# Performance work log

Hardware: AMD Instinct MI355X
Metric: run time of the kernel (lower is better)

The kernel has to match this reference:

```python
import jax, jax.numpy as jnp
import numpy as np

N, E, S, A, IN, H, OUT = 100000, 400000, 20000, 16, 32, 64, 1
NNZ_SS = 160000
CUR_T, CUR_W = 37, 3


def _gelu(x):
    return jax.nn.gelu(x, approximate=False)  # torch F.gelu default = exact erf


def _spmm(row, col, val, M, nseg):
    # sparse [nseg, K] (COO) @ dense M [K, H]
    return jax.ops.segment_sum(val[:, None] * M[col], row, num_segments=nseg)


def _seg_softmax(logits, seg, nseg):
    mx = jax.ops.segment_max(logits, seg, num_segments=nseg)
    mx = jnp.where(jnp.isfinite(mx), mx, 0.0)  # empty segments -> -inf
    ex = jnp.exp(logits - mx[seg])
    den = jax.ops.segment_sum(ex, seg, num_segments=nseg)
    return ex / (den[seg] + 1e-16)  # PyG softmax epsilon


def _gatv2(x, src, dst, eproj, Wl, bl, Wr, br, att, bias, n):
    # PyG GATv2Conv, heads=1, share_weights=False, negative_slope=0.2
    xl = x @ Wl + bl
    xr = x @ Wr + br
    m = xl[src] + xr[dst] + eproj                      # [nnz, H]
    e = jax.nn.leaky_relu(m, 0.2)
    alpha = _seg_softmax(e @ att, dst, n)              # softmax over in-edges per dst
    return jax.ops.segment_sum(alpha[:, None] * xl[src], dst, num_segments=n) + bias


def _forward(fl, edge_index, se_row, se_col, sn_row, sn_col, ss_row, ss_col, cur_t, cur_w):
    (x_rec, attr, se_val, sn_val, ss_val,
     node_embed, edge_embed, segment_embed, time_embed, week_embed,
     node_lin_W, node_lin_b, attr1_W, attr1_b, attr2_W, attr2_b,
     c1_Wl, c1_bl, c1_Wr, c1_br, c1_We, c1_att, c1_bias,
     c2_Wl, c2_bl, c2_Wr, c2_br, c2_We, c2_att, c2_bias,
     c3_Wl, c3_bl, c3_Wr, c3_br, c3_We, c3_att, c3_bias,
     lin1_W, lin1_b, lin2_W, lin2_b, out_W, out_b) = fl
    src, dst = edge_index[0], edge_index[1]
    attr_f = attr @ attr1_W + attr1_b                  # shared edge feature [E, H]
    # conv1 stack over node_embed with GELU + residual-to-initial
    h = node_embed
    pre = h
    for l in range(3):
        ep = attr_f @ c1_We[l]
        h = _gelu(_gatv2(h, src, dst, ep, c1_Wl[l], c1_bl[l], c1_Wr[l], c1_br[l], c1_att[l], c1_bias[l], N)) + pre
    # conv2 stack over projected recent features
    nf = _gelu(x_rec @ node_lin_W + node_lin_b)
    pre = nf
    for l in range(3):
        ep = attr_f @ c2_We[l]
        nf = _gelu(_gatv2(nf, src, dst, ep, c2_Wl[l], c2_bl[l], c2_Wr[l], c2_br[l], c2_att[l], c2_bias[l], N)) + pre
    # sparse segment aggregations
    x1e = _spmm(se_row, se_col, se_val, edge_embed, S)
    x2e = _spmm(se_row, se_col, se_val, attr @ attr2_W + attr2_b, S)
    x1n = _spmm(sn_row, sn_col, sn_val, h, S)
    x2n = _spmm(sn_row, sn_col, sn_val, nf, S)
    t = jnp.tile(time_embed[cur_t][None, :], (S, 1))
    w = jnp.tile(week_embed[cur_w][None, :], (S, 1))
    xf = jnp.concatenate([segment_embed, x1e, x2e, x1n, x2n, t, w], axis=1)  # [S, 7H]
    # conv3 over segment graph, edge_dim=1 (sparse values as edge attr)
    ep3 = ss_val[:, None] @ c3_We                                            # [nnz_ss, H]
    xf_gnn = _gelu(_gatv2(xf, ss_row, ss_col, ep3, c3_Wl, c3_bl, c3_Wr, c3_br, c3_att, c3_bias, S))
    # MLP head uses only lins[:-1] (as in the source)
    y = _gelu(xf @ lin1_W + lin1_b)
    y = _gelu(y @ lin2_W + lin2_b)
    out = jax.nn.sigmoid(jnp.concatenate([y, xf_gnn], axis=1) @ out_W + out_b) * 3600.0
    return out


def setup_inputs():
    key = jax.random.key(0)
    ks = jax.random.split(key, 64)
    it = iter(range(64))
    def nk():
        return ks[next(it)]
    def p(shape, s=0.05):
        return jax.random.normal(nk(), shape, jnp.float32) * s
    d = {}
    d["x_rec"] = jax.random.normal(nk(), (N, IN), jnp.float32)
    d["attr"] = jax.random.normal(nk(), (E, A), jnp.float32)
    d["se_val"] = jax.random.uniform(nk(), (E,), jnp.float32)
    d["sn_val"] = jax.random.uniform(nk(), (E,), jnp.float32)
    d["ss_val"] = jax.random.uniform(nk(), (NNZ_SS,), jnp.float32)
    d["node_embed"] = p((N, H))
    d["edge_embed"] = p((E, H))
    d["segment_embed"] = p((S, H))
    d["time_embed"] = p((96, H))
    d["week_embed"] = p((7, H))
    d["node_lin_W"] = p((IN, H)); d["node_lin_b"] = p((H,))
    d["attr1_W"] = p((A, H)); d["attr1_b"] = p((H,))
    d["attr2_W"] = p((A, H)); d["attr2_b"] = p((H,))
    for c in ("c1", "c2"):
        d[c + "_Wl"] = p((3, H, H)); d[c + "_bl"] = p((3, H))
        d[c + "_Wr"] = p((3, H, H)); d[c + "_br"] = p((3, H))
        d[c + "_We"] = p((3, H, H))
        d[c + "_att"] = p((3, H)); d[c + "_bias"] = p((3, H))
    d["c3_Wl"] = p((7 * H, H)); d["c3_bl"] = p((H,))
    d["c3_Wr"] = p((7 * H, H)); d["c3_br"] = p((H,))
    d["c3_We"] = p((1, H))
    d["c3_att"] = p((H,)); d["c3_bias"] = p((H,))
    d["lin1_W"] = p((7 * H, H)); d["lin1_b"] = p((H,))
    d["lin2_W"] = p((H, H)); d["lin2_b"] = p((H,))
    d["out_W"] = p((2 * H, OUT)); d["out_b"] = p((OUT,))
    d["edge_index"] = jax.random.randint(nk(), (2, E), 0, N)
    d["se_row"] = jax.random.randint(nk(), (E,), 0, S)
    d["se_col"] = jax.random.randint(nk(), (E,), 0, E)
    d["sn_row"] = jax.random.randint(nk(), (E,), 0, S)
    d["sn_col"] = jax.random.randint(nk(), (E,), 0, N)
    d["ss_row"] = jax.random.randint(nk(), (NNZ_SS,), 0, S)
    d["ss_col"] = jax.random.randint(nk(), (NNZ_SS,), 0, S)
    d["cur_t"] = CUR_T
    d["cur_w"] = CUR_W
    return d


def reference(x_rec, attr, se_val, sn_val, ss_val, node_embed, edge_embed, segment_embed, time_embed, week_embed, node_lin_W, node_lin_b, attr1_W, attr1_b, attr2_W, attr2_b, c1_Wl, c1_bl, c1_Wr, c1_br, c1_We, c1_att, c1_bias, c2_Wl, c2_bl, c2_Wr, c2_br, c2_We, c2_att, c2_bias, c3_Wl, c3_bl, c3_Wr, c3_br, c3_We, c3_att, c3_bias, lin1_W, lin1_b, lin2_W, lin2_b, out_W, out_b, edge_index, se_row, se_col, sn_row, sn_col, ss_row, ss_col, cur_t, cur_w):
    fl = (x_rec, attr, se_val, sn_val, ss_val, node_embed, edge_embed, segment_embed, time_embed, week_embed, node_lin_W, node_lin_b, attr1_W, attr1_b, attr2_W, attr2_b, c1_Wl, c1_bl, c1_Wr, c1_br, c1_We, c1_att, c1_bias, c2_Wl, c2_bl, c2_Wr, c2_br, c2_We, c2_att, c2_bias, c3_Wl, c3_bl, c3_Wr, c3_br, c3_We, c3_att, c3_bias, lin1_W, lin1_b, lin2_W, lin2_b, out_W, out_b)
    return _forward(fl, edge_index, se_row, se_col, sn_row, sn_col, ss_row, ss_col, cur_t, cur_w)
```

## Files before the change

kernel.cpp:

```cpp
#include <hip/hip_runtime.h>
#include <hip/hip_bf16.h>
#include <math.h>

#define DEV __device__ __forceinline__
typedef unsigned short u16;
typedef unsigned int u32;
typedef __attribute__((ext_vector_type(8))) short bf16x8;
typedef __attribute__((ext_vector_type(4))) float f32x4;

DEV float gelu_f(float x) { return 0.5f * x * (1.f + erff(x * 0.70710678118654752f)); }
DEV int rfl(int v) { return __builtin_amdgcn_readfirstlane(v); }
DEV float rflf(float v) {
  int i = __builtin_amdgcn_readfirstlane(__float_as_int(v));
  return __int_as_float(i);
}
DEV u16 f2b(float x) { __hip_bfloat16 h = __float2bfloat16(x); return *reinterpret_cast<u16*>(&h); }
DEV float b2f(u16 u) { __hip_bfloat16 h; *reinterpret_cast<u16*>(&h) = u; return __bfloat162float(h); }
DEV u32 pack2(float a, float b) { return (u32)f2b(a) | ((u32)f2b(b) << 16); }

__global__ void fill_zero(float* __restrict__ p, long n) {
  long i = (long)blockIdx.x * blockDim.x + threadIdx.x;
  long st = (long)gridDim.x * blockDim.x;
  for (; i < n; i += st) p[i] = 0.f;
}

__global__ void cvt_bf16(const float* __restrict__ src, u16* __restrict__ dst, long n) {
  long i = (long)blockIdx.x * blockDim.x + threadIdx.x;
  long st = (long)gridDim.x * blockDim.x;
  for (; i < n; i += st) dst[i] = f2b(src[i]);
}

__global__ void hist4_k(const int* __restrict__ k1, const int* __restrict__ k2,
                        const int* __restrict__ k3, const int* __restrict__ k4,
                        int E, int Z,
                        int* __restrict__ c1, int* __restrict__ c2,
                        int* __restrict__ c3, int* __restrict__ c4) {
  long total = 3L * E + Z;
  long i = (long)blockIdx.x * blockDim.x + threadIdx.x;
  long st = (long)gridDim.x * blockDim.x;
  for (; i < total; i += st) {
    if (i < E)               atomicAdd(&c1[k1[i]], 1);
    else if (i < 2L * E)     atomicAdd(&c2[k2[i - E]], 1);
    else if (i < 3L * E)     atomicAdd(&c3[k3[i - 2L * E]], 1);
    else                     atomicAdd(&c4[k4[i - 3L * E]], 1);
  }
}

__global__ __launch_bounds__(256) void scan_p1f(
    const int* __restrict__ c1, const int* __restrict__ c2,
    const int* __restrict__ c3, const int* __restrict__ c4,
    int n1, int nS, int nb1, int nbS,
    int* __restrict__ b1, int* __restrict__ b2,
    int* __restrict__ b3, int* __restrict__ b4) {
  int blk = blockIdx.x;
  const int* cnt; int* bsum; int n; int lb;
  if (blk < nb1)                { cnt = c1; bsum = b1; n = n1; lb = blk; }
  else if (blk < nb1 + nbS)     { cnt = c2; bsum = b2; n = nS; lb = blk - nb1; }
  else if (blk < nb1 + 2 * nbS) { cnt = c3; bsum = b3; n = nS; lb = blk - nb1 - nbS; }
  else                          { cnt = c4; bsum = b4; n = nS; lb = blk - nb1 - 2 * nbS; }
  __shared__ int ts[256];
  int base = lb * 1024;
  int s = 0;
  #pragma unroll
  for (int k = 0; k < 4; ++k) {
    int g = base + threadIdx.x * 4 + k;
    if (g < n) s += cnt[g];
  }
  ts[threadIdx.x] = s;
  __syncthreads();
  for (int d = 128; d; d >>= 1) {
    if (threadIdx.x < d) ts[threadIdx.x] += ts[threadIdx.x + d];
    __syncthreads();
  }
  if (threadIdx.x == 0) bsum[lb] = ts[0];
}

__global__ __launch_bounds__(256) void scan_p2f(
    int* __restrict__ b1, int* __restrict__ b2, int* __restrict__ b3, int* __restrict__ b4,
    int nb1, int nbS,
    int* __restrict__ rp1, int* __restrict__ rp2, int* __restrict__ rp3, int* __restrict__ rp4,
    int n1, int nS) {
  int g = blockIdx.x;
  int* bsum = g == 0 ? b1 : g == 1 ? b2 : g == 2 ? b3 : b4;
  int* rp   = g == 0 ? rp1 : g == 1 ? rp2 : g == 2 ? rp3 : rp4;
  int nb    = g == 0 ? nb1 : nbS;
  int n     = g == 0 ? n1 : nS;
  __shared__ int ts[256];
  int tid = threadIdx.x;
  int v = (tid < nb) ? bsum[tid] : 0;
  ts[tid] = v;
  __syncthreads();
  for (int d = 1; d < 256; d <<= 1) {
    int w = (tid >= d) ? ts[tid - d] : 0;
    __syncthreads();
    ts[tid] += w;
    __syncthreads();
  }
  if (tid < nb) bsum[tid] = (tid == 0) ? 0 : ts[tid - 1];
  if (tid == 255) rp[n] = ts[255];
}

__global__ __launch_bounds__(256) void scan_p3f(
    const int* __restrict__ c1, const int* __restrict__ c2,
    const int* __restrict__ c3, const int* __restrict__ c4,
    int n1, int nS, int nb1, int nbS,
    const int* __restrict__ b1, const int* __restrict__ b2,
    const int* __restrict__ b3, const int* __restrict__ b4,
    int* __restrict__ rp1, int* __restrict__ rp2,
    int* __restrict__ rp3, int* __restrict__ rp4,
    int* __restrict__ q1, int* __restrict__ q2,
    int* __restrict__ q3, int* __restrict__ q4) {
  int blk = blockIdx.x;
  const int* cnt; const int* bsum; int* rp; int* cursor; int n; int lb;
  if (blk < nb1)                { cnt = c1; bsum = b1; rp = rp1; cursor = q1; n = n1; lb = blk; }
  else if (blk < nb1 + nbS)     { cnt = c2; bsum = b2; rp = rp2; cursor = q2; n = nS; lb = blk - nb1; }
  else if (blk < nb1 + 2 * nbS) { cnt = c3; bsum = b3; rp = rp3; cursor = q3; n = nS; lb = blk - nb1 - nbS; }
  else                          { cnt = c4; bsum = b4; rp = rp4; cursor = q4; n = nS; lb = blk - nb1 - 2 * nbS; }
  __shared__ int ts[256];
  int base = lb * 1024;
  int tid = threadIdx.x;
  int c[4];
  int s = 0;
  #pragma unroll
  for (int k = 0; k < 4; ++k) {
    int g = base + tid * 4 + k;
    c[k] = (g < n) ? cnt[g] : 0;
    s += c[k];
  }
  ts[tid] = s;
  __syncthreads();
  for (int d = 1; d < 256; d <<= 1) {
    int w = (tid >= d) ? ts[tid - d] : 0;
    __syncthreads();
    ts[tid] += w;
    __syncthreads();
  }
  int run = bsum[lb] + ((tid == 0) ? 0 : ts[tid - 1]);
  #pragma unroll
  for (int k = 0; k < 4; ++k) {
    int g = base + tid * 4 + k;
    if (g < n) {
      rp[g] = run;
      cursor[g] = run;
      run += c[k];
    }
  }
}

__global__ void scat4_k(
    const int* __restrict__ edst, const int* __restrict__ esrc,
    const int* __restrict__ se_row, const int* __restrict__ se_col, const float* __restrict__ se_val,
    const int* __restrict__ sn_row, const int* __restrict__ sn_col, const float* __restrict__ sn_val,
    const int* __restrict__ ss_col, const int* __restrict__ ss_row, const float* __restrict__ ss_val,
    int E, int Z,
    int* __restrict__ q1, int* __restrict__ q2, int* __restrict__ q3, int* __restrict__ q4,
    int* __restrict__ src1s, int* __restrict__ eid1,
    int* __restrict__ col2s, float* __restrict__ val2s,
    int* __restrict__ col3s, float* __restrict__ val3s,
    int* __restrict__ src4s, float* __restrict__ val4s) {
  long total = 3L * E + Z;
  long i = (long)blockIdx.x * blockDim.x + threadIdx.x;
  long st = (long)gridDim.x * blockDim.x;
  for (; i < total; i += st) {
    if (i < E) {
      int p = atomicAdd(&q1[edst[i]], 1);
      src1s[p] = esrc[i]; eid1[p] = (int)i;
    } else if (i < 2L * E) {
      long j = i - E;
      int p = atomicAdd(&q2[se_row[j]], 1);
      col2s[p] = se_col[j]; val2s[p] = se_val[j];
    } else if (i < 3L * E) {
      long j = i - 2L * E;
      int p = atomicAdd(&q3[sn_row[j]], 1);
      col3s[p] = sn_col[j]; val3s[p] = sn_val[j];
    } else {
      long j = i - 3L * E;
      int p = atomicAdd(&q4[ss_col[j]], 1);
      src4s[p] = ss_row[j]; val4s[p] = ss_val[j];
    }
  }
}

__global__ __launch_bounds__(256) void compose_we(
    const float* __restrict__ a1W, const float* __restrict__ a1b,
    const float* __restrict__ c1We, const float* __restrict__ c2We,
    float* __restrict__ WEC, float* __restrict__ BEC)
{
  int l = blockIdx.x;
  const float* We = (l < 3) ? (c1We + l * 4096) : (c2We + (l - 3) * 4096);
  __shared__ float wes[4096];
  int tid = threadIdx.x;
  for (int i = tid; i < 4096; i += 256) wes[i] = We[i];
  __syncthreads();
  for (int i = tid; i < 1024; i += 256) {
    int k = i >> 6, j = i & 63;
    float s = 0.f;
    #pragma unroll 16
    for (int m = 0; m < 64; ++m) s += a1W[k * 64 + m] * wes[m * 64 + j];
    WEC[l * 1024 + i] = s;
  }
  if (tid < 64) {
    float s = 0.f;
    for (int m = 0; m < 64; ++m) s += a1b[m] * wes[m * 64 + tid];
    BEC[l * 64 + tid] = s;
  }
}

__global__ __launch_bounds__(256) void prep_wt(
    const float* __restrict__ c1Wl, const float* __restrict__ c1Wr,
    const float* __restrict__ c2Wl, const float* __restrict__ c2Wr,
    const float* __restrict__ nodeW, const float* __restrict__ c3Wl,
    const float* __restrict__ c3Wr, const float* __restrict__ lin1W,
    const float* __restrict__ lin2W, u16* __restrict__ WTS)
{
  long idx = (long)blockIdx.x * 256 + threadIdx.x;
  if (idx >= 141312) return;
  float v;
  if (idx < 49152) {
    const float* src = (idx < 12288) ? c1Wl : (idx < 24576) ? c1Wr : (idx < 36864) ? c2Wl : c2Wr;
    long loc = idx & 12287;
    long m = loc >> 12;
    int c = (int)((loc >> 6) & 63), k = (int)(loc & 63);
    v = src[m * 4096 + k * 64 + c];
  } else if (idx < 51200) {
    long loc = idx - 49152;
    int c = (int)(loc >> 5), k = (int)(loc & 31);
    v = nodeW[k * 64 + c];
  } else if (idx < 137216) {
    long base = (idx < 79872) ? 51200 : (idx < 108544) ? 79872 : 108544;
    const float* src = (idx < 79872) ? c3Wl : (idx < 108544) ? c3Wr : lin1W;
    long loc = idx - base;
    int c = (int)(loc / 448), k = (int)(loc % 448);
    v = src[k * 64 + c];
  } else {
    long loc = idx - 137216;
    int c = (int)(loc >> 6), k = (int)(loc & 63);
    v = lin2W[k * 64 + c];
  }
  WTS[idx] = f2b(v);
}

template <int ACT, bool PAIR, bool XBF, bool OBF, bool DUAL>
__global__ __launch_bounds__(256) void gemm_mfma(
    const void* __restrict__ Xv, int nrows, int K,
    const u16* __restrict__ WT1, const float* __restrict__ b1, void* __restrict__ O1v,
    const u16* __restrict__ WT2, const float* __restrict__ b2, void* __restrict__ O2v,
    const void* __restrict__ Xv2,
    const u16* __restrict__ WT3, const float* __restrict__ b3, void* __restrict__ O3v,
    const u16* __restrict__ WT4, const float* __restrict__ b4, void* __restrict__ O4v)
{
  __shared__ __align__(16) u16 xs[4096];
  __shared__ __align__(16) u16 ws1[4096];
  __shared__ __align__(16) u16 ws2[PAIR ? 4096 : 8];

  int bid = blockIdx.x;
  const void* X_ = Xv;
  const u16* w1p = WT1; const float* b1p = b1; void* o1p = O1v;
  const u16* w2p = WT2; const float* b2p = b2; void* o2p = O2v;
  if constexpr (DUAL) {
    int half = gridDim.x >> 1;
    if (bid >= half) {
      bid -= half;
      X_ = Xv2;
      w1p = WT3; b1p = b3; o1p = O3v;
      w2p = WT4; b2p = b4; o2p = O4v;
    }
  }

  const int tid = threadIdx.x;
  const int row0 = bid * 64;
  const int wid = tid >> 6, lane = tid & 63;
  const int lrow = lane & 15, lgrp = lane >> 4;
  const int r0 = wid * 16;
  const int sr = tid >> 2;
  const int sq = tid & 3;
  const int ssw = sr & 7;

  f32x4 acc[4];
  f32x4 acc2[PAIR ? 4 : 1];
  #pragma unroll
  for (int f = 0; f < 4; ++f) { acc[f] = (f32x4)0.f; if constexpr (PAIR) acc2[f] = (f32x4)0.f; }

  for (int kc = 0; kc < K; kc += 64) {
    __syncthreads();
    {
      int gr = row0 + sr;
      int kb = kc + sq * 16;
      uint4 pa, pb;
      if constexpr (XBF) {
        const u16* X = (const u16*)X_;
        if (gr < nrows && kb + 16 <= K) {
          pa = *(const uint4*)&X[(size_t)gr * K + kb];
          pb = *(const uint4*)&X[(size_t)gr * K + kb + 8];
        } else {
          u32 p[8];
          #pragma unroll
          for (int i = 0; i < 8; ++i) {
            u16 a = (gr < nrows && kb + 2 * i < K)     ? X[(size_t)gr * K + kb + 2 * i]     : (u16)0;
            u16 b = (gr < nrows && kb + 2 * i + 1 < K) ? X[(size_t)gr * K + kb + 2 * i + 1] : (u16)0;
            p[i] = (u32)a | ((u32)b << 16);
          }
          pa = make_uint4(p[0], p[1], p[2], p[3]);
          pb = make_uint4(p[4], p[5], p[6], p[7]);
        }
      } else {
        const float* X = (const float*)X_;
        float f[16];
        if (gr < nrows && kb + 16 <= K) {
          #pragma unroll
          for (int i = 0; i < 4; ++i)
            *(float4*)&f[i * 4] = *(const float4*)&X[(size_t)gr * K + kb + i * 4];
        } else {
          #pragma unroll
          for (int i = 0; i < 16; ++i)
            f[i] = (gr < nrows && kb + i < K) ? X[(size_t)gr * K + kb + i] : 0.f;
        }
        u32 p[8];
        #pragma unroll
        for (int i = 0; i < 8; ++i) p[i] = pack2(f[2 * i], f[2 * i + 1]);
        pa = make_uint4(p[0], p[1], p[2], p[3]);
        pb = make_uint4(p[4], p[5], p[6], p[7]);
      }
      *(uint4*)&xs[sr * 64 + (((sq * 2))     ^ ssw) * 8] = pa;
      *(uint4*)&xs[sr * 64 + (((sq * 2 + 1)) ^ ssw) * 8] = pb;
    }
    {
      int kb = kc + sq * 16;
      uint4 qa, qb;
      if (kb + 16 <= K) {
        qa = *(const uint4*)&w1p[(size_t)sr * K + kb];
        qb = *(const uint4*)&w1p[(size_t)sr * K + kb + 8];
      } else {
        u32 p[8];
        #pragma unroll
        for (int i = 0; i < 8; ++i) {
          u16 a = (kb + 2 * i < K)     ? w1p[(size_t)sr * K + kb + 2 * i]     : (u16)0;
          u16 b = (kb + 2 * i + 1 < K) ? w1p[(size_t)sr * K + kb + 2 * i + 1] : (u16)0;
          p[i] = (u32)a | ((u32)b << 16);
        }
        qa = make_uint4(p[0], p[1], p[2], p[3]);
        qb = make_uint4(p[4], p[5], p[6], p[7]);
      }
      *(uint4*)&ws1[sr * 64 + (((sq * 2))     ^ ssw) * 8] = qa;
      *(uint4*)&ws1[sr * 64 + (((sq * 2 + 1)) ^ ssw) * 8] = qb;
      if constexpr (PAIR) {
        if (kb + 16 <= K) {
          qa = *(const uint4*)&w2p[(size_t)sr * K + kb];
          qb = *(const uint4*)&w2p[(size_t)sr * K + kb + 8];
        } else {
          u32 p[8];
          #pragma unroll
          for (int i = 0; i < 8; ++i) {
            u16 a = (kb + 2 * i < K)     ? w2p[(size_t)sr * K + kb + 2 * i]     : (u16)0;
            u16 b = (kb + 2 * i + 1 < K) ? w2p[(size_t)sr * K + kb + 2 * i + 1] : (u16)0;
            p[i] = (u32)a | ((u32)b << 16);
          }
          qa = make_uint4(p[0], p[1], p[2], p[3]);
          qb = make_uint4(p[4], p[5], p[6], p[7]);
        }
        *(uint4*)&ws2[sr * 64 + (((sq * 2))     ^ ssw) * 8] = qa;
        *(uint4*)&ws2[sr * 64 + (((sq * 2 + 1)) ^ ssw) * 8] = qb;
      }
    }
    __syncthreads();
    #pragma unroll
    for (int kh = 0; kh < 2; ++kh) {
      const int g = (4 * kh + lgrp) ^ (lrow & 7);
      bf16x8 a = *(const bf16x8*)&xs[(r0 + lrow) * 64 + g * 8];
      #pragma unroll
      for (int f = 0; f < 4; ++f) {
        int col = f * 16 + lrow;
        bf16x8 b = *(const bf16x8*)&ws1[col * 64 + g * 8];
        acc[f] = __builtin_amdgcn_mfma_f32_16x16x32_bf16(a, b, acc[f], 0, 0, 0);
        if constexpr (PAIR) {
          bf16x8 b2v = *(const bf16x8*)&ws2[col * 64 + g * 8];
          acc2[f] = __builtin_amdgcn_mfma_f32_16x16x32_bf16(a, b2v, acc2[f], 0, 0, 0);
        }
      }
    }
  }

  #pragma unroll
  for (int f = 0; f < 4; ++f) {
    int col = f * 16 + lrow;
    float bv = b1p[col];
    float bv2 = 0.f;
    if constexpr (PAIR) bv2 = b2p[col];
    #pragma unroll
    for (int r = 0; r < 4; ++r) {
      int grow = row0 + r0 + lgrp * 4 + r;
      if (grow >= nrows) continue;
      float v = acc[f][r] + bv;
      if constexpr (ACT == 1) v = gelu_f(v);
      if constexpr (OBF) ((u16*)o1p)[(size_t)grow * 64 + col] = f2b(v);
      else               ((float*)o1p)[(size_t)grow * 64 + col] = v;
      if constexpr (PAIR) {
        float v2 = acc2[f][r] + bv2;
        if constexpr (ACT == 1) v2 = gelu_f(v2);
        if constexpr (OBF) ((u16*)o2p)[(size_t)grow * 64 + col] = f2b(v2);
        else               ((float*)o2p)[(size_t)grow * 64 + col] = v2;
      }
    }
  }
}

__global__ __launch_bounds__(256) void gat_gather2(
    const int* __restrict__ rowptr, const int* __restrict__ eids,
    const int* __restrict__ srcs, const float* __restrict__ attr,
    const float* __restrict__ wec1, const float* __restrict__ bec1,
    const float* __restrict__ att1, const float* __restrict__ bias1,
    const float* __restrict__ wec2, const float* __restrict__ bec2,
    const float* __restrict__ att2, const float* __restrict__ bias2,
    const u16* __restrict__ xl1, const u16* __restrict__ xr1,
    const u16* __restrict__ pre1, u16* __restrict__ out1,
    const u16* __restrict__ xl2, const u16* __restrict__ xr2,
    const u16* __restrict__ pre2, u16* __restrict__ out2, int n)
{
  int tid = threadIdx.x;
  int wid = tid >> 6, lane = tid & 63;
  int d = blockIdx.x * 4 + wid;
  if (d >= n) return;
  float w1[16], w2[16];
  #pragma unroll
  for (int k = 0; k < 16; ++k) {
    w1[k] = wec1[k * 64 + lane];
    w2[k] = wec2[k * 64 + lane];
  }
  float be1 = bec1[lane], be2 = bec2[lane];
  float at1 = att1[lane], at2 = att2[lane];
  float xr1v = b2f(xr1[(size_t)d * 64 + lane]);
  float xr2v = b2f(xr2[(size_t)d * 64 + lane]);
  float n1 = 0.f, d1 = 0.f, n2 = 0.f, d2 = 0.f;
  int j0 = rfl(rowptr[d]), j1 = rfl(rowptr[d + 1]);
  int j = j0;
  for (; j + 2 <= j1; j += 2) {
    int ea = rfl(eids[j]),     sa = rfl(srcs[j]);
    int eb = rfl(eids[j + 1]), sb = rfl(srcs[j + 1]);
    const float* ara = attr + (size_t)ea * 16;
    const float* arb = attr + (size_t)eb * 16;
    float xl1a = b2f(xl1[(size_t)sa * 64 + lane]);
    float xl2a = b2f(xl2[(size_t)sa * 64 + lane]);
    float xl1b = b2f(xl1[(size_t)sb * 64 + lane]);
    float xl2b = b2f(xl2[(size_t)sb * 64 + lane]);
    float ep1a = be1, ep2a = be2, ep1b = be1, ep2b = be2;
    #pragma unroll
    for (int k = 0; k < 16; ++k) {
      float aka = ara[k], akb = arb[k];
      ep1a += aka * w1[k]; ep2a += aka * w2[k];
      ep1b += akb * w1[k]; ep2b += akb * w2[k];
    }
    float m1a = xl1a + xr1v + ep1a, m2a = xl2a + xr2v + ep2a;
    float m1b = xl1b + xr1v + ep1b, m2b = xl2b + xr2v + ep2b;
    float l1a = m1a < 0.f ? 0.2f * m1a : m1a;
    float l2a = m2a < 0.f ? 0.2f * m2a : m2a;
    float l1b = m1b < 0.f ? 0.2f * m1b : m1b;
    float l2b = m2b < 0.f ? 0.2f * m2b : m2b;
    float t1a = at1 * l1a, t2a = at2 * l2a, t1b = at1 * l1b, t2b = at2 * l2b;
    #pragma unroll
    for (int o = 32; o; o >>= 1) {
      t1a += __shfl_xor(t1a, o, 64);
      t2a += __shfl_xor(t2a, o, 64);
      t1b += __shfl_xor(t1b, o, 64);
      t2b += __shfl_xor(t2b, o, 64);
    }
    float x1a = __expf(t1a), x2a = __expf(t2a), x1b = __expf(t1b), x2b = __expf(t2b);
    n1 += x1a * xl1a + x1b * xl1b; d1 += x1a + x1b;
    n2 += x2a * xl2a + x2b * xl2b; d2 += x2a + x2b;
  }
  for (; j < j1; ++j) {
    int e = rfl(eids[j]);
    int s = rfl(srcs[j]);
    const float* arow = attr + (size_t)e * 16;
    float xl1v = b2f(xl1[(size_t)s * 64 + lane]);
    float xl2v = b2f(xl2[(size_t)s * 64 + lane]);
    float ep1 = be1, ep2 = be2;
    #pragma unroll
    for (int k = 0; k < 16; ++k) {
      float ak = arow[k];
      ep1 += ak * w1[k];
      ep2 += ak * w2[k];
    }
    float m1 = xl1v + xr1v + ep1;
    float m2 = xl2v + xr2v + ep2;
    float lr1 = m1 < 0.f ? 0.2f * m1 : m1;
    float lr2 = m2 < 0.f ? 0.2f * m2 : m2;
    float t1 = at1 * lr1, t2 = at2 * lr2;
    #pragma unroll
    for (int o = 32; o; o >>= 1) {
      t1 += __shfl_xor(t1, o, 64);
      t2 += __shfl_xor(t2, o, 64);
    }
    float ex1 = __expf(t1), ex2 = __expf(t2);
    n1 += ex1 * xl1v; d1 += ex1;
    n2 += ex2 * xl2v; d2 += ex2;
  }
  size_t base = (size_t)d * 64 + lane;
  float v1 = n1 / (d1 + 1e-16f) + bias1[lane];
  float v2 = n2 / (d2 + 1e-16f) + bias2[lane];
  out1[base] = f2b(gelu_f(v1) + b2f(pre1[base]));
  out2[base] = f2b(gelu_f(v2) + b2f(pre2[base]));
}

__global__ __launch_bounds__(256) void gat_seg_g(
    const int* __restrict__ rowptr, const int* __restrict__ srcs,
    const float* __restrict__ vals,
    const float* __restrict__ we3, const float* __restrict__ att,
    const float* __restrict__ bias,
    const u16* __restrict__ xl, const u16* __restrict__ xr,
    float* __restrict__ out, int n)
{
  int tid = threadIdx.x;
  int wid = tid >> 6, lane = tid & 63;
  int d0 = (blockIdx.x * 4 + wid) * 4;
  if (d0 >= n) return;
  float we3v = we3[lane], attv = att[lane], bsv = bias[lane];
  int dend = min(d0 + 4, n);
  for (int d = d0; d < dend; ++d) {
    float xrv = b2f(xr[(size_t)d * 64 + lane]);
    float accn = 0.f, accd = 0.f;
    int j0 = rfl(rowptr[d]), j1 = rfl(rowptr[d + 1]);
    for (int j = j0; j < j1; ++j) {
      int s = rfl(srcs[j]);
      float vv = rflf(vals[j]);
      float ep = vv * we3v;
      float xlv = b2f(xl[(size_t)s * 64 + lane]);
      float m = xlv + xrv + ep;
      float lr = m < 0.f ? 0.2f * m : m;
      float t = attv * lr;
      #pragma unroll
      for (int o = 32; o; o >>= 1) t += __shfl_xor(t, o, 64);
      float ex = __expf(t);
      accn += ex * xlv;
      accd += ex;
    }
    float v = accn / (accd + 1e-16f) + bsv;
    out[(size_t)d * 64 + lane] = gelu_f(v);
  }
}

__global__ __launch_bounds__(256) void xf_build(
    const int* __restrict__ rp2, const int* __restrict__ col2s, const float* __restrict__ val2s,
    const int* __restrict__ rp3, const int* __restrict__ col3s, const float* __restrict__ val3s,
    const float* __restrict__ edge_embed, const float* __restrict__ attr,
    const float* __restrict__ W2, const float* __restrict__ b2,
    const float* __restrict__ seg_embed, const float* __restrict__ time_embed,
    const float* __restrict__ week_embed,
    const int* __restrict__ cur_t, const int* __restrict__ cur_w,
    const u16* __restrict__ h, const u16* __restrict__ nf,
    float* __restrict__ xf, int S)
{
  __shared__ float ws[1024];
  __shared__ float bs[64];
  int tid = threadIdx.x;
  for (int i = tid; i < 1024; i += 256) ws[i] = W2[i];
  if (tid < 64) bs[tid] = b2[tid];
  __syncthreads();
  int wid = tid >> 6, lane = tid & 63;
  int s0 = (blockIdx.x * 4 + wid) * 4;
  if (s0 >= S) return;
  float te = time_embed[cur_t[0] * 64 + lane];
  float we = week_embed[cur_w[0] * 64 + lane];
  int send = min(s0 + 4, S);
  for (int s = s0; s < send; ++s) {
    float* row = xf + (size_t)s * 448;
    row[lane]       = seg_embed[(size_t)s * 64 + lane];
    row[320 + lane] = te;
    row[384 + lane] = we;
    float acc1 = 0.f, aat = 0.f, vs = 0.f;
    int j0 = rfl(rp2[s]), j1 = rfl(rp2[s + 1]);
    for (int j = j0; j < j1; ++j) {
      int c = rfl(col2s[j]);
      float v = rflf(val2s[j]);
      acc1 += v * edge_embed[(size_t)c * 64 + lane];
      aat  += v * attr[(size_t)c * 16 + (lane & 15)];
      vs   += v;
    }
    float x2 = vs * bs[lane];
    #pragma unroll
    for (int k = 0; k < 16; ++k)
      x2 += __shfl(aat, k, 64) * ws[k * 64 + lane];
    row[64 + lane]  = acc1;
    row[128 + lane] = x2;
    float acch = 0.f, accf = 0.f;
    j0 = rfl(rp3[s]); j1 = rfl(rp3[s + 1]);
    for (int j = j0; j < j1; ++j) {
      int c = rfl(col3s[j]);
      float v = rflf(val3s[j]);
      acch += v * b2f(h[(size_t)c * 64 + lane]);
      accf += v * b2f(nf[(size_t)c * 64 + lane]);
    }
    row[192 + lane] = acch;
    row[256 + lane] = accf;
  }
}

__global__ __launch_bounds__(256) void head_k(
    const float* __restrict__ y2, const float* __restrict__ xfg,
    const float* __restrict__ outW, const float* __restrict__ outb,
    float* __restrict__ out, int S)
{
  int wid = threadIdx.x >> 6, lane = threadIdx.x & 63;
  int s = blockIdx.x * 4 + wid;
  if (s >= S) return;
  float t = y2[(size_t)s * 64 + lane] * outW[lane] + xfg[(size_t)s * 64 + lane] * outW[64 + lane];
  #pragma unroll
  for (int o = 32; o; o >>= 1) t += __shfl_xor(t, o, 64);
  if (lane == 0) {
    float z = t + outb[0];
    out[s] = 3600.f / (1.f + __expf(-z));
  }
}

extern "C" void kernel_launch(void* const* d_in, const int* in_sizes, int n_in,
                              void* d_out, int out_size, void* d_ws, size_t ws_size,
                              hipStream_t stream)
{
  const float* x_rec       = (const float*)d_in[0];
  const float* attr        = (const float*)d_in[1];
  const float* se_val      = (const float*)d_in[2];
  const float* sn_val      = (const float*)d_in[3];
  const float* ss_val      = (const float*)d_in[4];
  const float* node_embed  = (const float*)d_in[5];
  const float* edge_embed  = (const float*)d_in[6];
  const float* seg_embed   = (const float*)d_in[7];
  const float* time_embed  = (const float*)d_in[8];
  const float* week_embed  = (const float*)d_in[9];
  const float* node_lin_W  = (const float*)d_in[10];
  const float* node_lin_b  = (const float*)d_in[11];
  const float* attr2_W     = (const float*)d_in[14];
  const float* attr2_b     = (const float*)d_in[15];
  const float* c1_Wl       = (const float*)d_in[16];
  const float* c1_bl       = (const float*)d_in[17];
  const float* c1_Wr       = (const float*)d_in[18];
  const float* c1_br       = (const float*)d_in[19];
  const float* c1_att      = (const float*)d_in[21];
  const float* c1_bias     = (const float*)d_in[22];
  const float* c2_Wl       = (const float*)d_in[23];
  const float* c2_bl       = (const float*)d_in[24];
  const float* c2_Wr       = (const float*)d_in[25];
  const float* c2_br       = (const float*)d_in[26];
  const float* c2_att      = (const float*)d_in[28];
  const float* c2_bias     = (const float*)d_in[29];
  const float* c3_Wl       = (const float*)d_in[30];
  const float* c3_bl       = (const float*)d_in[31];
  const float* c3_Wr       = (const float*)d_in[32];
  const float* c3_br       = (const float*)d_in[33];
  const float* c3_We       = (const float*)d_in[34];
  const float* c3_att      = (const float*)d_in[35];
  const float* c3_bias     = (const float*)d_in[36];
  const float* lin1_W      = (const float*)d_in[37];
  const float* lin1_b      = (const float*)d_in[38];
  const float* lin2_W      = (const float*)d_in[39];
  const float* lin2_b      = (const float*)d_in[40];
  const float* out_W       = (const float*)d_in[41];
  const float* out_b       = (const float*)d_in[42];
  const int* edge_index    = (const int*)d_in[43];
  const int* se_row        = (const int*)d_in[44];
  const int* se_col        = (const int*)d_in[45];
  const int* sn_row        = (const int*)d_in[46];
  const int* sn_col        = (const int*)d_in[47];
  const int* ss_row        = (const int*)d_in[48];
  const int* ss_col        = (const int*)d_in[49];
  const int* cur_t         = (const int*)d_in[50];
  const int* cur_w         = (const int*)d_in[51];

  const int N = in_sizes[0] / 32;
  const int E = in_sizes[1] / 16;
  const int S = in_sizes[7] / 64;
  const int NNZSS = in_sizes[4];

  float* W = (float*)d_ws;
  size_t o = 0;
  u16* A   = (u16*)(W + o); o += (size_t)N * 32;
  u16* B   = (u16*)(W + o); o += (size_t)N * 32;
  u16* A2  = (u16*)(W + o); o += (size_t)N * 32;
  u16* B2  = (u16*)(W + o); o += (size_t)N * 32;
  u16* Hc  = (u16*)(W + o); o += (size_t)N * 32;
  u16* F0  = (u16*)(W + o); o += (size_t)N * 32;
  u16* Fc  = (u16*)(W + o); o += (size_t)N * 32;
  u16* NE  = (u16*)(W + o); o += (size_t)N * 32;
  float* XF  = W + o; o += (size_t)S * 448;
  float* XFG = W + o; o += (size_t)S * 64;
  float* Y   = W + o; o += (size_t)S * 64;
  float* Y2  = W + o; o += (size_t)S * 64;
  float* WEC = W + o; o += 6 * 1024;
  float* BEC = W + o; o += 6 * 64;
  u16* WTS   = (u16*)(W + o); o += 70656;
  float* val2s = W + o; o += E;
  float* val3s = W + o; o += E;
  float* val4s = W + o; o += NNZSS;
  int* I = (int*)(W + o);
  size_t q = 0;
  int* cur1 = I + q; q += N + 1;
  int* cur2 = I + q; q += S + 1;
  int* cur3 = I + q; q += S + 1;
  int* cur4 = I + q; q += S + 1;
  int* rp1  = I + q; q += N + 1;
  int* rp2  = I + q; q += S + 1;
  int* rp3  = I + q; q += S + 1;
  int* rp4  = I + q; q += S + 1;
  int* eid1  = I + q; q += E;
  int* src1s = I + q; q += E;
  int* col2s = I + q; q += E;
  int* col3s = I + q; q += E;
  int* src4s = I + q; q += NNZSS;
  int* bs1  = I + q; q += 256;
  int* bs2  = I + q; q += 256;
  int* bs3  = I + q; q += 256;
  int* bs4  = I + q; q += 256;

  u16* WT_c1l  = WTS;
  u16* WT_c1r  = WTS + 12288;
  u16* WT_c2l  = WTS + 24576;
  u16* WT_c2r  = WTS + 36864;
  u16* WT_node = WTS + 49152;
  u16* WT_c3l  = WTS + 51200;
  u16* WT_c3r  = WTS + 79872;
  u16* WT_lin1 = WTS + 108544;
  u16* WT_lin2 = WTS + 137216;

  const int* edst = edge_index + E;

  dim3 blk(256);
  const int gN64 = (N + 63) / 64;
  const int gS64 = (S + 63) / 64;
  const int gS4  = (S + 3) / 4;
  const int gN4  = (N + 3) / 4;
  const int gSeg = (S + 15) / 16;
  const int nbN  = (N + 1 + 1023) / 1024;
  const int nbS  = (S + 1 + 1023) / 1024;

  long ztot = (long)(N + 1) + 3L * (S + 1);
  fill_zero<<<256, blk, 0, stream>>>((float*)cur1, ztot);
  prep_wt<<<(141312 + 255) / 256, blk, 0, stream>>>(c1_Wl, c1_Wr, c2_Wl, c2_Wr,
                                                    node_lin_W, c3_Wl, c3_Wr,
                                                    lin1_W, lin2_W, WTS);
  cvt_bf16<<<1024, blk, 0, stream>>>(node_embed, NE, (long)N * 64);
  hist4_k<<<1024, blk, 0, stream>>>(edst, se_row, sn_row, ss_col, E, NNZSS,
                                    cur1, cur2, cur3, cur4);
  scan_p1f<<<nbN + 3 * nbS, blk, 0, stream>>>(cur1, cur2, cur3, cur4,
                                              N + 1, S + 1, nbN, nbS,
                                              bs1, bs2, bs3, bs4);
  scan_p2f<<<4, blk, 0, stream>>>(bs1, bs2, bs3, bs4, nbN, nbS,
                                  rp1, rp2, rp3, rp4, N, S);
  scan_p3f<<<nbN + 3 * nbS, blk, 0, stream>>>(cur1, cur2, cur3, cur4,
                                              N, S, nbN, nbS,
                                              bs1, bs2, bs3, bs4,
                                              rp1, rp2, rp3, rp4,
                                              cur1, cur2, cur3, cur4);
  scat4_k<<<1024, blk, 0, stream>>>(edst, edge_index,
                                    se_row, se_col, se_val,
                                    sn_row, sn_col, sn_val,
                                    ss_col, ss_row, ss_val,
                                    E, NNZSS,
                                    cur1, cur2, cur3, cur4,
                                    src1s, eid1, col2s, val2s, col3s, val3s, src4s, val4s);

  compose_we<<<6, blk, 0, stream>>>((const float*)d_in[12], (const float*)d_in[13],
                                    (const float*)d_in[20], (const float*)d_in[27], WEC, BEC);

  gemm_mfma<1, false, false, true, false><<<gN64, blk, 0, stream>>>(x_rec, N, 32,
      WT_node, node_lin_b, F0, nullptr, nullptr, nullptr,
      nullptr, nullptr, nullptr, nullptr, nullptr, nullptr, nullptr);

  for (int l = 0; l < 3; ++l) {
    gemm_mfma<0, true, true, true, true><<<2 * gN64, blk, 0, stream>>>(
        l == 0 ? NE : Hc, N, 64,
        WT_c1l + l * 4096, c1_bl + l * 64, A, WT_c1r + l * 4096, c1_br + l * 64, B,
        l == 0 ? F0 : Fc,
        WT_c2l + l * 4096, c2_bl + l * 64, A2, WT_c2r + l * 4096, c2_br + l * 64, B2);
    gat_gather2<<<gN4, blk, 0, stream>>>(rp1, eid1, src1s, attr,
        WEC + l * 1024, BEC + l * 64, c1_att + l * 64, c1_bias + l * 64,
        WEC + (3 + l) * 1024, BEC + (3 + l) * 64, c2_att + l * 64, c2_bias + l * 64,
        A, B, NE, Hc,
        A2, B2, F0, Fc, N);
  }

  xf_build<<<gSeg, blk, 0, stream>>>(rp2, col2s, val2s, rp3, col3s, val3s,
                                     edge_embed, attr, attr2_W, attr2_b,
                                     seg_embed, time_embed, week_embed, cur_t, cur_w,
                                     Hc, Fc, XF, S);

  gemm_mfma<0, true, false, true, false><<<gS64, blk, 0, stream>>>(XF, S, 448,
      WT_c3l, c3_bl, A, WT_c3r, c3_br, B,
      nullptr, nullptr, nullptr, nullptr, nullptr, nullptr, nullptr);
  gat_seg_g<<<gSeg, blk, 0, stream>>>(rp4, src4s, val4s, c3_We, c3_att, c3_bias,
                                      A, B, XFG, S);

  gemm_mfma<1, false, false, false, false><<<gS64, blk, 0, stream>>>(XF, S, 448,
      WT_lin1, lin1_b, Y, nullptr, nullptr, nullptr,
      nullptr, nullptr, nullptr, nullptr, nullptr, nullptr, nullptr);
  gemm_mfma<1, false, false, false, false><<<gS64, blk, 0, stream>>>(Y, S, 64,
      WT_lin2, lin2_b, Y2, nullptr, nullptr, nullptr,
      nullptr, nullptr, nullptr, nullptr, nullptr, nullptr, nullptr);
  head_k<<<gS4, blk, 0, stream>>>(Y2, XFG, out_W, out_b, (float*)d_out, S);
}
```

Measured before the change: 703.7 us.

## Pre-sort edge attrs into CSR order as bf16 and widen segment kernel parallelism

Edge attributes are packed into bf16 in destination-sorted CSR order during the scatter pass, so the three GAT gather passes read them contiguously instead of through an eid indirection on fp32 rows. Edge embeddings are converted to bf16 alongside node embeddings so the segment feature build reads half the bytes. The xf_build kernel splits each segment's work across two wavefronts, and both it and gat_seg_g move from four segments per wave to one, to raise parallelism. The trade-off is extra conversion and scatter work up front plus bf16 rounding of attrs and edge embeddings.

```diff
diff --git a/kernel.cpp b/kernel.cpp
--- a/kernel.cpp
+++ b/kernel.cpp
@@ -17,6 +17,8 @@
 DEV u16 f2b(float x) { __hip_bfloat16 h = __float2bfloat16(x); return *reinterpret_cast<u16*>(&h); }
 DEV float b2f(u16 u) { __hip_bfloat16 h; *reinterpret_cast<u16*>(&h) = u; return __bfloat162float(h); }
 DEV u32 pack2(float a, float b) { return (u32)f2b(a) | ((u32)f2b(b) << 16); }
+DEV float blo(u32 u) { return __int_as_float((int)(u << 16)); }
+DEV float bhi(u32 u) { return __int_as_float((int)(u & 0xffff0000u)); }
 
 __global__ void fill_zero(float* __restrict__ p, long n) {
   long i = (long)blockIdx.x * blockDim.x + threadIdx.x;
@@ -24,10 +26,16 @@
   for (; i < n; i += st) p[i] = 0.f;
 }
 
-__global__ void cvt_bf16(const float* __restrict__ src, u16* __restrict__ dst, long n) {
+__global__ void cvt_all(const float* __restrict__ ne, const float* __restrict__ ee,
+                        u16* __restrict__ NE, u16* __restrict__ EE,
+                        long nNE, long nEE) {
+  long total = nNE + nEE;
   long i = (long)blockIdx.x * blockDim.x + threadIdx.x;
   long st = (long)gridDim.x * blockDim.x;
-  for (; i < n; i += st) dst[i] = f2b(src[i]);
+  for (; i < total; i += st) {
+    if (i < nNE) NE[i] = f2b(ne[i]);
+    else         EE[i - nNE] = f2b(ee[i - nNE]);
+  }
 }
 
 __global__ void hist4_k(const int* __restrict__ k1, const int* __restrict__ k2,
@@ -149,12 +157,13 @@
 
 __global__ void scat4_k(
     const int* __restrict__ edst, const int* __restrict__ esrc,
+    const float* __restrict__ attr,
     const int* __restrict__ se_row, const int* __restrict__ se_col, const float* __restrict__ se_val,
     const int* __restrict__ sn_row, const int* __restrict__ sn_col, const float* __restrict__ sn_val,
     const int* __restrict__ ss_col, const int* __restrict__ ss_row, const float* __restrict__ ss_val,
     int E, int Z,
     int* __restrict__ q1, int* __restrict__ q2, int* __restrict__ q3, int* __restrict__ q4,
-    int* __restrict__ src1s, int* __restrict__ eid1,
+    int* __restrict__ src1s, u16* __restrict__ atrs,
     int* __restrict__ col2s, float* __restrict__ val2s,
     int* __restrict__ col3s, float* __restrict__ val3s,
     int* __restrict__ src4s, float* __restrict__ val4s) {
@@ -164,7 +173,11 @@
   for (; i < total; i += st) {
     if (i < E) {
       int p = atomicAdd(&q1[edst[i]], 1);
-      src1s[p] = esrc[i]; eid1[p] = (int)i;
+      src1s[p] = esrc[i];
+      const float* sr = attr + (size_t)i * 16;
+      u32* dr = (u32*)(atrs + (size_t)p * 16);
+      #pragma unroll
+      for (int k = 0; k < 8; ++k) dr[k] = pack2(sr[2 * k], sr[2 * k + 1]);
     } else if (i < 2L * E) {
       long j = i - E;
       int p = atomicAdd(&q2[se_row[j]], 1);
@@ -405,8 +418,8 @@
 }
 
 __global__ __launch_bounds__(256) void gat_gather2(
-    const int* __restrict__ rowptr, const int* __restrict__ eids,
-    const int* __restrict__ srcs, const float* __restrict__ attr,
+    const int* __restrict__ rowptr,
+    const int* __restrict__ srcs, const u16* __restrict__ atrs,
     const float* __restrict__ wec1, const float* __restrict__ bec1,
     const float* __restrict__ att1, const float* __restrict__ bias1,
     const float* __restrict__ wec2, const float* __restrict__ bec2,
@@ -434,20 +447,24 @@
   int j0 = rfl(rowptr[d]), j1 = rfl(rowptr[d + 1]);
   int j = j0;
   for (; j + 2 <= j1; j += 2) {
-    int ea = rfl(eids[j]),     sa = rfl(srcs[j]);
-    int eb = rfl(eids[j + 1]), sb = rfl(srcs[j + 1]);
-    const float* ara = attr + (size_t)ea * 16;
-    const float* arb = attr + (size_t)eb * 16;
+    int sa = rfl(srcs[j]);
+    int sb = rfl(srcs[j + 1]);
+    const u32* ara = (const u32*)(atrs + (size_t)j * 16);
+    const u32* arb = ara + 8;
     float xl1a = b2f(xl1[(size_t)sa * 64 + lane]);
     float xl2a = b2f(xl2[(size_t)sa * 64 + lane]);
     float xl1b = b2f(xl1[(size_t)sb * 64 + lane]);
     float xl2b = b2f(xl2[(size_t)sb * 64 + lane]);
     float ep1a = be1, ep2a = be2, ep1b = be1, ep2b = be2;
     #pragma unroll
-    for (int k = 0; k < 16; ++k) {
-      float aka = ara[k], akb = arb[k];
-      ep1a += aka * w1[k]; ep2a += aka * w2[k];
-      ep1b += akb * w1[k]; ep2b += akb * w2[k];
+    for (int k = 0; k < 8; ++k) {
+      u32 pa_ = ara[k], pb_ = arb[k];
+      float a0 = blo(pa_), a1 = bhi(pa_);
+      float b0 = blo(pb_), b1 = bhi(pb_);
+      ep1a += a0 * w1[2 * k] + a1 * w1[2 * k + 1];
+      ep2a += a0 * w2[2 * k] + a1 * w2[2 * k + 1];
+      ep1b += b0 * w1[2 * k] + b1 * w1[2 * k + 1];
+      ep2b += b0 * w2[2 * k] + b1 * w2[2 * k + 1];
     }
     float m1a = xl1a + xr1v + ep1a, m2a = xl2a + xr2v + ep2a;
     float m1b = xl1b + xr1v + ep1b, m2b = xl2b + xr2v + ep2b;
@@ -468,17 +485,17 @@
     n2 += x2a * xl2a + x2b * xl2b; d2 += x2a + x2b;
   }
   for (; j < j1; ++j) {
-    int e = rfl(eids[j]);
     int s = rfl(srcs[j]);
-    const float* arow = attr + (size_t)e * 16;
+    const u32* arow = (const u32*)(atrs + (size_t)j * 16);
     float xl1v = b2f(xl1[(size_t)s * 64 + lane]);
     float xl2v = b2f(xl2[(size_t)s * 64 + lane]);
     float ep1 = be1, ep2 = be2;
     #pragma unroll
-    for (int k = 0; k < 16; ++k) {
-      float ak = arow[k];
-      ep1 += ak * w1[k];
-      ep2 += ak * w2[k];
+    for (int k = 0; k < 8; ++k) {
+      u32 pk = arow[k];
+      float a0 = blo(pk), a1 = bhi(pk);
+      ep1 += a0 * w1[2 * k] + a1 * w1[2 * k + 1];
+      ep2 += a0 * w2[2 * k] + a1 * w2[2 * k + 1];
     }
     float m1 = xl1v + xr1v + ep1;
     float m2 = xl2v + xr2v + ep2;
@@ -511,37 +528,34 @@
 {
   int tid = threadIdx.x;
   int wid = tid >> 6, lane = tid & 63;
-  int d0 = (blockIdx.x * 4 + wid) * 4;
-  if (d0 >= n) return;
+  int d = blockIdx.x * 4 + wid;
+  if (d >= n) return;
   float we3v = we3[lane], attv = att[lane], bsv = bias[lane];
-  int dend = min(d0 + 4, n);
-  for (int d = d0; d < dend; ++d) {
-    float xrv = b2f(xr[(size_t)d * 64 + lane]);
-    float accn = 0.f, accd = 0.f;
-    int j0 = rfl(rowptr[d]), j1 = rfl(rowptr[d + 1]);
-    for (int j = j0; j < j1; ++j) {
-      int s = rfl(srcs[j]);
-      float vv = rflf(vals[j]);
-      float ep = vv * we3v;
-      float xlv = b2f(xl[(size_t)s * 64 + lane]);
-      float m = xlv + xrv + ep;
-      float lr = m < 0.f ? 0.2f * m : m;
-      float t = attv * lr;
-      #pragma unroll
-      for (int o = 32; o; o >>= 1) t += __shfl_xor(t, o, 64);
-      float ex = __expf(t);
-      accn += ex * xlv;
-      accd += ex;
-    }
-    float v = accn / (accd + 1e-16f) + bsv;
-    out[(size_t)d * 64 + lane] = gelu_f(v);
-  }
+  float xrv = b2f(xr[(size_t)d * 64 + lane]);
+  float accn = 0.f, accd = 0.f;
+  int j0 = rfl(rowptr[d]), j1 = rfl(rowptr[d + 1]);
+  for (int j = j0; j < j1; ++j) {
+    int s = rfl(srcs[j]);
+    float vv = rflf(vals[j]);
+    float ep = vv * we3v;
+    float xlv = b2f(xl[(size_t)s * 64 + lane]);
+    float m = xlv + xrv + ep;
+    float lr = m < 0.f ? 0.2f * m : m;
+    float t = attv * lr;
+    #pragma unroll
+    for (int o = 32; o; o >>= 1) t += __shfl_xor(t, o, 64);
+    float ex = __expf(t);
+    accn += ex * xlv;
+    accd += ex;
+  }
+  float v = accn / (accd + 1e-16f) + bsv;
+  out[(size_t)d * 64 + lane] = gelu_f(v);
 }
 
 __global__ __launch_bounds__(256) void xf_build(
     const int* __restrict__ rp2, const int* __restrict__ col2s, const float* __restrict__ val2s,
     const int* __restrict__ rp3, const int* __restrict__ col3s, const float* __restrict__ val3s,
-    const float* __restrict__ edge_embed, const float* __restrict__ attr,
+    const u16* __restrict__ EE, const float* __restrict__ attr,
     const float* __restrict__ W2, const float* __restrict__ b2,
     const float* __restrict__ seg_embed, const float* __restrict__ time_embed,
     const float* __restrict__ week_embed,
@@ -556,22 +570,20 @@
   if (tid < 64) bs[tid] = b2[tid];
   __syncthreads();
   int wid = tid >> 6, lane = tid & 63;
-  int s0 = (blockIdx.x * 4 + wid) * 4;
-  if (s0 >= S) return;
-  float te = time_embed[cur_t[0] * 64 + lane];
-  float we = week_embed[cur_w[0] * 64 + lane];
-  int send = min(s0 + 4, S);
-  for (int s = s0; s < send; ++s) {
-    float* row = xf + (size_t)s * 448;
+  int gw = blockIdx.x * 4 + wid;
+  int s = gw >> 1, role = gw & 1;
+  if (s >= S) return;
+  float* row = xf + (size_t)s * 448;
+  if (role == 0) {
     row[lane]       = seg_embed[(size_t)s * 64 + lane];
-    row[320 + lane] = te;
-    row[384 + lane] = we;
+    row[320 + lane] = time_embed[cur_t[0] * 64 + lane];
+    row[384 + lane] = week_embed[cur_w[0] * 64 + lane];
     float acc1 = 0.f, aat = 0.f, vs = 0.f;
     int j0 = rfl(rp2[s]), j1 = rfl(rp2[s + 1]);
     for (int j = j0; j < j1; ++j) {
       int c = rfl(col2s[j]);
       float v = rflf(val2s[j]);
-      acc1 += v * edge_embed[(size_t)c * 64 + lane];
+      acc1 += v * b2f(EE[(size_t)c * 64 + lane]);
       aat  += v * attr[(size_t)c * 16 + (lane & 15)];
       vs   += v;
     }
@@ -581,8 +593,9 @@
       x2 += __shfl(aat, k, 64) * ws[k * 64 + lane];
     row[64 + lane]  = acc1;
     row[128 + lane] = x2;
+  } else {
     float acch = 0.f, accf = 0.f;
-    j0 = rfl(rp3[s]); j1 = rfl(rp3[s + 1]);
+    int j0 = rfl(rp3[s]), j1 = rfl(rp3[s + 1]);
     for (int j = j0; j < j1; ++j) {
       int c = rfl(col3s[j]);
       float v = rflf(val3s[j]);
@@ -679,6 +692,8 @@
   u16* F0  = (u16*)(W + o); o += (size_t)N * 32;
   u16* Fc  = (u16*)(W + o); o += (size_t)N * 32;
   u16* NE  = (u16*)(W + o); o += (size_t)N * 32;
+  u16* EE  = (u16*)(W + o); o += (size_t)E * 32;
+  u16* ATRS = (u16*)(W + o); o += (size_t)E * 8;
   float* XF  = W + o; o += (size_t)S * 448;
   float* XFG = W + o; o += (size_t)S * 64;
   float* Y   = W + o; o += (size_t)S * 64;
@@ -699,7 +714,6 @@
   int* rp2  = I + q; q += S + 1;
   int* rp3  = I + q; q += S + 1;
   int* rp4  = I + q; q += S + 1;
-  int* eid1  = I + q; q += E;
   int* src1s = I + q; q += E;
   int* col2s = I + q; q += E;
   int* col3s = I + q; q += E;
@@ -726,7 +740,7 @@
   const int gS64 = (S + 63) / 64;
   const int gS4  = (S + 3) / 4;
   const int gN4  = (N + 3) / 4;
-  const int gSeg = (S + 15) / 16;
+  const int gXF  = (2 * S + 3) / 4;
   const int nbN  = (N + 1 + 1023) / 1024;
   const int nbS  = (S + 1 + 1023) / 1024;
 
@@ -735,7 +749,8 @@
   prep_wt<<<(141312 + 255) / 256, blk, 0, stream>>>(c1_Wl, c1_Wr, c2_Wl, c2_Wr,
                                                     node_lin_W, c3_Wl, c3_Wr,
                                                     lin1_W, lin2_W, WTS);
-  cvt_bf16<<<1024, blk, 0, stream>>>(node_embed, NE, (long)N * 64);
+  cvt_all<<<2048, blk, 0, stream>>>(node_embed, edge_embed, NE, EE,
+                                    (long)N * 64, (long)E * 64);
   hist4_k<<<1024, blk, 0, stream>>>(edst, se_row, sn_row, ss_col, E, NNZSS,
                                     cur1, cur2, cur3, cur4);
   scan_p1f<<<nbN + 3 * nbS, blk, 0, stream>>>(cur1, cur2, cur3, cur4,
@@ -748,13 +763,13 @@
                                               bs1, bs2, bs3, bs4,
                                               rp1, rp2, rp3, rp4,
                                               cur1, cur2, cur3, cur4);
-  scat4_k<<<1024, blk, 0, stream>>>(edst, edge_index,
+  scat4_k<<<1024, blk, 0, stream>>>(edst, edge_index, attr,
                                     se_row, se_col, se_val,
                                     sn_row, sn_col, sn_val,
                                     ss_col, ss_row, ss_val,
                                     E, NNZSS,
                                     cur1, cur2, cur3, cur4,
-                                    src1s, eid1, col2s, val2s, col3s, val3s, src4s, val4s);
+                                    src1s, ATRS, col2s, val2s, col3s, val3s, src4s, val4s);
 
   compose_we<<<6, blk, 0, stream>>>((const float*)d_in[12], (const float*)d_in[13],
                                     (const float*)d_in[20], (const float*)d_in[27], WEC, BEC);
@@ -769,23 +784,23 @@
         WT_c1l + l * 4096, c1_bl + l * 64, A, WT_c1r + l * 4096, c1_br + l * 64, B,
         l == 0 ? F0 : Fc,
         WT_c2l + l * 4096, c2_bl + l * 64, A2, WT_c2r + l * 4096, c2_br + l * 64, B2);
-    gat_gather2<<<gN4, blk, 0, stream>>>(rp1, eid1, src1s, attr,
+    gat_gather2<<<gN4, blk, 0, stream>>>(rp1, src1s, ATRS,
         WEC + l * 1024, BEC + l * 64, c1_att + l * 64, c1_bias + l * 64,
         WEC + (3 + l) * 1024, BEC + (3 + l) * 64, c2_att + l * 64, c2_bias + l * 64,
         A, B, NE, Hc,
         A2, B2, F0, Fc, N);
   }
 
-  xf_build<<<gSeg, blk, 0, stream>>>(rp2, col2s, val2s, rp3, col3s, val3s,
-                                     edge_embed, attr, attr2_W, attr2_b,
-                                     seg_embed, time_embed, week_embed, cur_t, cur_w,
-                                     Hc, Fc, XF, S);
+  xf_build<<<gXF, blk, 0, stream>>>(rp2, col2s, val2s, rp3, col3s, val3s,
+                                    EE, attr, attr2_W, attr2_b,
+                                    seg_embed, time_embed, week_embed, cur_t, cur_w,
+                                    Hc, Fc, XF, S);
 
   gemm_mfma<0, true, false, true, false><<<gS64, blk, 0, stream>>>(XF, S, 448,
       WT_c3l, c3_bl, A, WT_c3r, c3_br, B,
       nullptr, nullptr, nullptr, nullptr, nullptr, nullptr, nullptr);
-  gat_seg_g<<<gSeg, blk, 0, stream>>>(rp4, src4s, val4s, c3_We, c3_att, c3_bias,
-                                      A, B, XFG, S);
+  gat_seg_g<<<gS4, blk, 0, stream>>>(rp4, src4s, val4s, c3_We, c3_att, c3_bias,
+                                     A, B, XFG, S);
 
   gemm_mfma<1, false, false, false, false><<<gS64, blk, 0, stream>>>(XF, S, 448,
       WT_lin1, lin1_b, Y, nullptr, nullptr, nullptr,
```

After: 736.8 us. 1.05x slower.
